# Kernel tuning notes

Hardware: AMD Instinct MI355X
Metric: run time of the kernel (lower is better)

The kernel has to match this reference:

```python
import jax, jax.numpy as jnp
import numpy as np
from jax import lax

N = 512  # neurons (== input features in this base class)

@jax.custom_vjp
def spike_fn(x):
    # Heaviside spike with fast-sigmoid surrogate gradient (standard for LIF SNNs)
    return (x > 0.0).astype(x.dtype)

def _spike_fwd(x):
    return spike_fn(x), x

def _spike_bwd(x, g):
    sg = 1.0 / (1.0 + 10.0 * jnp.abs(x)) ** 2
    return (g * sg,)

spike_fn.defvjp(_spike_fwd, _spike_bwd)

def setup_inputs() -> dict:
    key = jax.random.key(0)
    k1, k2, k3, k4, k5, k6 = jax.random.split(key, 6)
    B, T = 64, 1000
    scale = 1.0 / np.sqrt(N)
    return {
        "input_batch": jax.random.normal(k1, (B, T, N), dtype=jnp.float32),
        "state_snn": jnp.zeros((2, B, N), dtype=jnp.float32),  # [v; s]
        "state_LI": jnp.zeros((B, N), dtype=jnp.float32),
        "W1": jax.random.normal(k2, (N, N), dtype=jnp.float32) * scale,
        "W2": jax.random.normal(k3, (N, N), dtype=jnp.float32) * scale,
        "leak_v": jax.random.uniform(k4, (N,), dtype=jnp.float32, minval=0.8, maxval=0.99),
        "leak_i": jax.random.uniform(k5, (N,), dtype=jnp.float32, minval=0.8, maxval=0.99),
        "thresh": jax.random.uniform(k6, (N,), dtype=jnp.float32, minval=0.5, maxval=1.5),
    }

def reference(input_batch, state_snn, state_LI, W1, W2, leak_v, leak_i, thresh):
    # input_batch: [B, T, N]; time loop expressed as lax.scan over T
    v0, s0 = state_snn[0], state_snn[1]
    xs = jnp.swapaxes(input_batch, 0, 1)  # [T, B, N]

    def step(carry, x_t):
        v, s, u = carry
        ff = x_t @ W1.T                        # LIF feed-forward current
        v = leak_v * v * (1.0 - s) + ff        # leak + reset-to-zero on spike
        s = spike_fn(v - thresh)               # spike generation
        u = leak_i * u + s @ W2.T              # leaky-integrator readout
        return (v, s, u), (s, jnp.stack([v, s]), u)

    _, (spikes, states_snn, decoded) = lax.scan(step, (v0, s0, state_LI), xs)
    # spikes: [T,B,N], states_snn: [T,2,B,N], decoded: [T,B,N]
    return spikes, states_snn, decoded
```

## Files before the change

### kernel.cpp

```cpp
#include <hip/hip_runtime.h>

#define T_STEPS 1000
#define B_SZ 64
#define N_SZ 512
#define BN_TOT (B_SZ * N_SZ)
#define TBN   ((size_t)T_STEPS * BN_TOT)

typedef __attribute__((ext_vector_type(4))) float f32x4;
typedef __attribute__((ext_vector_type(8))) short bf16x8;
typedef unsigned short ushort_t;

__global__ __launch_bounds__(256, 2)
void sgemm_abt(const float* __restrict__ A, const float* __restrict__ W,
               float* __restrict__ C)
{
    constexpr int K = 512;
    constexpr int BK = 32;
    constexpr int LDT = 128 + 4;
    __shared__ float As[BK][LDT];
    __shared__ float Bs[BK][LDT];

    const int tid = threadIdx.x;
    const int tx = tid & 15;
    const int ty = tid >> 4;
    const size_t m0 = (size_t)blockIdx.y * 128;
    const int n0 = blockIdx.x * 128;

    float acc[8][8];
#pragma unroll
    for (int i = 0; i < 8; ++i)
#pragma unroll
        for (int j = 0; j < 8; ++j) acc[i][j] = 0.0f;

    for (int k0 = 0; k0 < K; k0 += BK) {
#pragma unroll
        for (int p = 0; p < 4; ++p) {
            int i = tid + p * 256;
            int r = i >> 3;
            int q = i & 7;
            float4 va = *(const float4*)(A + (m0 + r) * K + k0 + q * 4);
            As[q * 4 + 0][r] = va.x; As[q * 4 + 1][r] = va.y;
            As[q * 4 + 2][r] = va.z; As[q * 4 + 3][r] = va.w;
            float4 vb = *(const float4*)(W + (size_t)(n0 + r) * K + k0 + q * 4);
            Bs[q * 4 + 0][r] = vb.x; Bs[q * 4 + 1][r] = vb.y;
            Bs[q * 4 + 2][r] = vb.z; Bs[q * 4 + 3][r] = vb.w;
        }
        __syncthreads();
#pragma unroll
        for (int k = 0; k < BK; ++k) {
            float a[8], b[8];
            *(float4*)&a[0] = *(const float4*)&As[k][ty * 8];
            *(float4*)&a[4] = *(const float4*)&As[k][ty * 8 + 4];
            *(float4*)&b[0] = *(const float4*)&Bs[k][tx * 4];
            *(float4*)&b[4] = *(const float4*)&Bs[k][tx * 4 + 64];
#pragma unroll
            for (int i = 0; i < 8; ++i)
#pragma unroll
                for (int j = 0; j < 8; ++j)
                    acc[i][j] = fmaf(a[i], b[j], acc[i][j]);
        }
        __syncthreads();
    }

#pragma unroll
    for (int i = 0; i < 8; ++i) {
        float* cp = C + (m0 + ty * 8 + i) * 512 + n0 + tx * 4;
        *(float4*)cp        = make_float4(acc[i][0], acc[i][1], acc[i][2], acc[i][3]);
        *(float4*)(cp + 64) = make_float4(acc[i][4], acc[i][5], acc[i][6], acc[i][7]);
    }
}

__global__ __launch_bounds__(256)
void w2_split(const float* __restrict__ W2, ushort_t* __restrict__ Wc)
{
    int i = blockIdx.x * 256 + threadIdx.x;
    int n = i >> 9, k = i & 511;
    float w = W2[i];
    unsigned wb = __float_as_uint(w);
    float h = __uint_as_float(wb & 0xFFFF0000u);
    float r1 = w - h;
    unsigned r1b = __float_as_uint(r1);
    float m = __uint_as_float(r1b & 0xFFFF0000u);
    float r2 = r1 - m;
    size_t base = (size_t)n * 1536 + k;
    Wc[base]        = (ushort_t)(wb >> 16);
    Wc[base + 512]  = (ushort_t)(r1b >> 16);
    Wc[base + 1024] = (ushort_t)(__float_as_uint(r2) >> 16);
}

__global__ __launch_bounds__(256, 2)
void gemm2_mfma(const ushort_t* __restrict__ S, const ushort_t* __restrict__ Wc,
                float* __restrict__ C)
{
    __shared__ ushort_t As[128 * 32];
    __shared__ ushort_t Bs[128 * 32];

    const int tid = threadIdx.x;
    const int m0 = blockIdx.y * 128;
    const int n0 = blockIdx.x * 128;
    const int wid = tid >> 6;
    const int lane = tid & 63;
    const int wm = (wid >> 1) * 64;
    const int wn = (wid & 1) * 64;
    const int fr = lane & 15;
    const int fq = lane >> 4;

    f32x4 acc[4][4] = {};

    const int rA = tid >> 2;
    const int cA = (tid & 3) * 8;

    for (int k0 = 0; k0 < 1536; k0 += 32) {
        const int kk = k0 & 511;
#pragma unroll
        for (int i = 0; i < 2; ++i) {
            __builtin_amdgcn_global_load_lds(
                (const __attribute__((address_space(1))) unsigned int*)
                    (S + (size_t)(m0 + i * 64 + rA) * 512 + kk + cA),
                (__attribute__((address_space(3))) unsigned int*)
                    (As + i * 2048 + tid * 8),
                16, 0, 0);
            __builtin_amdgcn_global_load_lds(
                (const __attribute__((address_space(1))) unsigned int*)
                    (Wc + (size_t)(n0 + i * 64 + rA) * 1536 + k0 + cA),
                (__attribute__((address_space(3))) unsigned int*)
                    (Bs + i * 2048 + tid * 8),
                16, 0, 0);
        }
        asm volatile("s_waitcnt vmcnt(0)" ::: "memory");
        __syncthreads();

        bf16x8 a[4], b[4];
#pragma unroll
        for (int m = 0; m < 4; ++m)
            a[m] = *(const bf16x8*)(As + (wm + m * 16 + fr) * 32 + fq * 8);
#pragma unroll
        for (int n = 0; n < 4; ++n)
            b[n] = *(const bf16x8*)(Bs + (wn + n * 16 + fr) * 32 + fq * 8);
#pragma unroll
        for (int m = 0; m < 4; ++m)
#pragma unroll
            for (int n = 0; n < 4; ++n)
                acc[m][n] = __builtin_amdgcn_mfma_f32_16x16x32_bf16(
                    a[m], b[n], acc[m][n], 0, 0, 0);
        __syncthreads();
    }

#pragma unroll
    for (int m = 0; m < 4; ++m) {
        const int row = m0 + wm + m * 16 + fq * 4;
#pragma unroll
        for (int n = 0; n < 4; ++n) {
            const int col = n0 + wn + n * 16 + fr;
#pragma unroll
            for (int j = 0; j < 4; ++j)
                C[(size_t)(row + j) * 512 + col] = acc[m][n][j];
        }
    }
}

__global__ __launch_bounds__(128)
void lif_scan(const float* __restrict__ ff, const float* __restrict__ st0,
              const float* __restrict__ leak_v, const float* __restrict__ thresh,
              float* __restrict__ spikes, float* __restrict__ states,
              ushort_t* __restrict__ sbf)
{
    const int idx = blockIdx.x * 128 + threadIdx.x;
    const int n = idx & (N_SZ - 1);
    const int b = idx >> 9;

    float v = st0[idx];
    float s = st0[BN_TOT + idx];
    const float lv = leak_v[n];
    const float th = thresh[n];

    const float* fp = ff + (size_t)b * T_STEPS * N_SZ + n;
    float* sp  = spikes + idx;
    float* stp = states + idx;
    ushort_t* sbp = sbf ? (sbf + idx) : (ushort_t*)0;

    float f0 = fp[0], f1 = fp[N_SZ], f2 = fp[2 * N_SZ], f3 = fp[3 * N_SZ];

    for (int t = 0; t < T_STEPS; t += 4) {
        float g0 = 0.f, g1 = 0.f, g2 = 0.f, g3 = 0.f;
        if (t + 4 < T_STEPS) {
            const float* q = fp + (size_t)(t + 4) * N_SZ;
            g0 = q[0]; g1 = q[N_SZ]; g2 = q[2 * N_SZ]; g3 = q[3 * N_SZ];
        }
#define LIF_STEP(F, TOFF)                                                  \
        {                                                                  \
            v = lv * v * (1.0f - s) + (F);                                 \
            s = (v > th) ? 1.0f : 0.0f;                                    \
            size_t o  = (size_t)(t + (TOFF)) * BN_TOT;                     \
            size_t o2 = (size_t)(t + (TOFF)) * (2 * BN_TOT);               \
            sp[o] = s;                                                     \
            stp[o2] = v;                                                   \
            stp[o2 + BN_TOT] = s;                                          \
            if (sbp) sbp[o] = (ushort_t)(__float_as_uint(s) >> 16);        \
        }
        LIF_STEP(f0, 0) LIF_STEP(f1, 1) LIF_STEP(f2, 2) LIF_STEP(f3, 3)
#undef LIF_STEP
        f0 = g0; f1 = g1; f2 = g2; f3 = g3;
    }
}

__global__ __launch_bounds__(128)
void li_scan(float* __restrict__ dec, const float* __restrict__ u0,
             const float* __restrict__ leak_i)
{
    const int idx = blockIdx.x * 128 + threadIdx.x;
    const int n = idx & (N_SZ - 1);

    float u = u0[idx];
    const float li = leak_i[n];
    float* p = dec + idx;

    float y0 = p[0], y1 = p[BN_TOT], y2 = p[2 * (size_t)BN_TOT], y3 = p[3 * (size_t)BN_TOT];

    for (int t = 0; t < T_STEPS; t += 4) {
        float g0 = 0.f, g1 = 0.f, g2 = 0.f, g3 = 0.f;
        if (t + 4 < T_STEPS) {
            float* q = p + (size_t)(t + 4) * BN_TOT;
            g0 = q[0]; g1 = q[BN_TOT]; g2 = q[2 * (size_t)BN_TOT]; g3 = q[3 * (size_t)BN_TOT];
        }
#define LI_STEP(Y, TOFF)                                                   \
        {                                                                  \
            u = fmaf(li, u, (Y));                                          \
            p[(size_t)(t + (TOFF)) * BN_TOT] = u;                          \
        }
        LI_STEP(y0, 0) LI_STEP(y1, 1) LI_STEP(y2, 2) LI_STEP(y3, 3)
#undef LI_STEP
        y0 = g0; y1 = g1; y2 = g2; y3 = g3;
    }
}

extern "C" void kernel_launch(void* const* d_in, const int* in_sizes, int n_in,
                              void* d_out, int out_size, void* d_ws, size_t ws_size,
                              hipStream_t stream)
{
    (void)in_sizes; (void)n_in; (void)out_size;

    const float* X     = (const float*)d_in[0];
    const float* st_sn = (const float*)d_in[1];
    const float* st_li = (const float*)d_in[2];
    const float* W1    = (const float*)d_in[3];
    const float* W2    = (const float*)d_in[4];
    const float* lv    = (const float*)d_in[5];
    const float* li    = (const float*)d_in[6];
    const float* th    = (const float*)d_in[7];

    float* spikes = (float*)d_out;
    float* states = spikes + TBN;
    float* dec    = states + 2 * TBN;

    const size_t WS_NEED = (size_t)512 * 1536 * 2 + (size_t)64000 * 512 * 2;
    const bool use_mfma = (ws_size >= WS_NEED);
    ushort_t* Wc = (ushort_t*)d_ws;
    ushort_t* Sb = Wc + (size_t)512 * 1536;

    const dim3 gemm_grid(4, 500), gemm_block(256);
    const dim3 scan_grid(BN_TOT / 128), scan_block(128);

    if (use_mfma)
        w2_split<<<dim3(1024), dim3(256), 0, stream>>>(W2, Wc);

    sgemm_abt<<<gemm_grid, gemm_block, 0, stream>>>(X, W1, dec);

    lif_scan<<<scan_grid, scan_block, 0, stream>>>(dec, st_sn, lv, th,
                                                   spikes, states,
                                                   use_mfma ? Sb : nullptr);

    if (use_mfma)
        gemm2_mfma<<<gemm_grid, gemm_block, 0, stream>>>(Sb, Wc, dec);
    else
        sgemm_abt<<<gemm_grid, gemm_block, 0, stream>>>(spikes, W2, dec);

    li_scan<<<scan_grid, scan_block, 0, stream>>>(dec, st_li, li);
}
```

Before: 840.6 us.

## Drop third bf16 split term of W2 and double-buffer gemm2 LDS loads

The bf16 split of W2 goes from three terms (hi, mid, lo) to two, which shortens the K loop of the spike×W2 MFMA GEMM by a third. The GEMM also gains ping-pong LDS buffers, so the next tile's global-to-LDS load is issued before the current tile's MFMAs. This cuts MFMA work and hides part of the load latency. The cost is a larger approximation error on W2, roughly 16 mantissa bits instead of about 24, which could flip results near tolerance, plus twice the LDS per block.

Result: faster. 798.3 us (-5.0%).

```diff
diff --git a/kernel.cpp b/kernel.cpp
--- a/kernel.cpp
+++ b/kernel.cpp
@@ -80,20 +80,18 @@
     float h = __uint_as_float(wb & 0xFFFF0000u);
     float r1 = w - h;
     unsigned r1b = __float_as_uint(r1);
-    float m = __uint_as_float(r1b & 0xFFFF0000u);
-    float r2 = r1 - m;
-    size_t base = (size_t)n * 1536 + k;
-    Wc[base]        = (ushort_t)(wb >> 16);
-    Wc[base + 512]  = (ushort_t)(r1b >> 16);
-    Wc[base + 1024] = (ushort_t)(__float_as_uint(r2) >> 16);
+    size_t base = (size_t)n * 1024 + k;
+    Wc[base]       = (ushort_t)(wb >> 16);
+    Wc[base + 512] = (ushort_t)(r1b >> 16);
 }
 
 __global__ __launch_bounds__(256, 2)
 void gemm2_mfma(const ushort_t* __restrict__ S, const ushort_t* __restrict__ Wc,
                 float* __restrict__ C)
 {
-    __shared__ ushort_t As[128 * 32];
-    __shared__ ushort_t Bs[128 * 32];
+    constexpr int NT = 1024 / 32;
+    __shared__ ushort_t As[2][128 * 32];
+    __shared__ ushort_t Bs[2][128 * 32];
 
     const int tid = threadIdx.x;
     const int m0 = blockIdx.y * 128;
@@ -110,41 +108,55 @@
     const int rA = tid >> 2;
     const int cA = (tid & 3) * 8;
 
-    for (int k0 = 0; k0 < 1536; k0 += 32) {
-        const int kk = k0 & 511;
-#pragma unroll
-        for (int i = 0; i < 2; ++i) {
-            __builtin_amdgcn_global_load_lds(
-                (const __attribute__((address_space(1))) unsigned int*)
-                    (S + (size_t)(m0 + i * 64 + rA) * 512 + kk + cA),
-                (__attribute__((address_space(3))) unsigned int*)
-                    (As + i * 2048 + tid * 8),
-                16, 0, 0);
-            __builtin_amdgcn_global_load_lds(
-                (const __attribute__((address_space(1))) unsigned int*)
-                    (Wc + (size_t)(n0 + i * 64 + rA) * 1536 + k0 + cA),
-                (__attribute__((address_space(3))) unsigned int*)
-                    (Bs + i * 2048 + tid * 8),
-                16, 0, 0);
-        }
-        asm volatile("s_waitcnt vmcnt(0)" ::: "memory");
-        __syncthreads();
+#define STAGE(buf, t)                                                        \
+    {                                                                        \
+        const int k0_ = (t) * 32;                                            \
+        const int kk_ = k0_ & 511;         \
+        _Pragma("unroll")                                                    \
+        for (int i = 0; i < 2; ++i) {                                        \
+            __builtin_amdgcn_global_load_lds(                                \
+                (const __attribute__((address_space(1))) unsigned int*)      \
+                    (S + (size_t)(m0 + i * 64 + rA) * 512 + kk_ + cA),       \
+                (__attribute__((address_space(3))) unsigned int*)            \
+                    (As[buf] + i * 2048 + tid * 8),                          \
+                16, 0, 0);                                                   \
+            __builtin_amdgcn_global_load_lds(                                \
+                (const __attribute__((address_space(1))) unsigned int*)      \
+                    (Wc + (size_t)(n0 + i * 64 + rA) * 1024 + k0_ + cA),     \
+                (__attribute__((address_space(3))) unsigned int*)            \
+                    (Bs[buf] + i * 2048 + tid * 8),                          \
+                16, 0, 0);                                                   \
+        }                                                                    \
+    }
+
+    STAGE(0, 0);
+    asm volatile("s_waitcnt vmcnt(0)" ::: "memory");
+    __syncthreads();
+
+    int cur = 0;
+    for (int t = 0; t < NT; ++t) {
+        if (t + 1 < NT)
+            STAGE(cur ^ 1, t + 1);
 
         bf16x8 a[4], b[4];
 #pragma unroll
         for (int m = 0; m < 4; ++m)
-            a[m] = *(const bf16x8*)(As + (wm + m * 16 + fr) * 32 + fq * 8);
+            a[m] = *(const bf16x8*)(As[cur] + (wm + m * 16 + fr) * 32 + fq * 8);
 #pragma unroll
         for (int n = 0; n < 4; ++n)
-            b[n] = *(const bf16x8*)(Bs + (wn + n * 16 + fr) * 32 + fq * 8);
+            b[n] = *(const bf16x8*)(Bs[cur] + (wn + n * 16 + fr) * 32 + fq * 8);
 #pragma unroll
         for (int m = 0; m < 4; ++m)
 #pragma unroll
             for (int n = 0; n < 4; ++n)
                 acc[m][n] = __builtin_amdgcn_mfma_f32_16x16x32_bf16(
                     a[m], b[n], acc[m][n], 0, 0, 0);
+
+        asm volatile("s_waitcnt vmcnt(0)" ::: "memory");
         __syncthreads();
-    }
+        cur ^= 1;
+    }
+#undef STAGE
 
 #pragma unroll
     for (int m = 0; m < 4; ++m) {
@@ -253,10 +265,10 @@
     float* states = spikes + TBN;
     float* dec    = states + 2 * TBN;
 
-    const size_t WS_NEED = (size_t)512 * 1536 * 2 + (size_t)64000 * 512 * 2;
+    const size_t WS_NEED = (size_t)512 * 1024 * 2 + (size_t)64000 * 512 * 2;
     const bool use_mfma = (ws_size >= WS_NEED);
     ushort_t* Wc = (ushort_t*)d_ws;
-    ushort_t* Sb = Wc + (size_t)512 * 1536;
+    ushort_t* Sb = Wc + (size_t)512 * 1024;
 
     const dim3 gemm_grid(4, 500), gemm_block(256);
     const dim3 scan_grid(BN_TOT / 128), scan_block(128);
@@ -268,7 +280,7 @@
 
     lif_scan<<<scan_grid, scan_block, 0, stream>>>(dec, st_sn, lv, th,
                                                    spikes, states,
-                                                   use_mfma ? Sb : nullptr);
+                                                   use_mfma ? Sb : (ushort_t*)0);
 
     if (use_mfma)
         gemm2_mfma<<<gemm_grid, gemm_block, 0, stream>>>(Sb, Wc, dec);
```
